# Performance work log

Measured on AMD Instinct MI355X. Metric: run time of the kernel, lower is better.

## Reference

```python
import jax, jax.numpy as jnp
import numpy as np

LEN = 2048

def setup_inputs() -> dict:
    key = jax.random.key(0)
    k1, k2 = jax.random.split(key)
    x = jax.random.normal(k1, (LEN,), dtype=jnp.float32)
    y = jax.random.normal(k2, (LEN,), dtype=jnp.float32)
    return {"x": x, "y": y}

def reference(x, y):
    # Classic DTW DP with squared-difference cost.
    # Original torch code clamps indices with max(i-1,0)/max(j-1,0); because
    # DTW[i,j] is still +inf when read, the clamped reads reduce to the
    # standard recurrence: row 0 is a cumulative sum, col 0 uses only 'up',
    # interior uses min(up, left, diag).
    inf = jnp.float32(jnp.inf)
    cost0 = (x[0] - y) ** 2            # [len2]
    row0 = jnp.cumsum(cost0)           # DTW row i=0

    def row_step(prev_row, xi):
        cost = (xi - y) ** 2                                   # [len2]
        diag = jnp.concatenate([prev_row[:1], prev_row[:-1]])  # prev_row[j-1], clamped at j=0
        def cell(left, cud):
            c, up, dg = cud
            v = c + jnp.minimum(jnp.minimum(up, left), dg)
            return v, v
        # left init = inf => at j=0 min reduces to min(up, diag) = prev_row[0]
        _, new_row = jax.lax.scan(cell, inf, (cost, prev_row, diag))
        return new_row, None

    last_row, _ = jax.lax.scan(row_step, row0, x[1:])
    return jnp.sqrt(last_row[-1])
```

## Files before the change

kernel.cpp:

```cpp
#include <hip/hip_runtime.h>
#include <math.h>


#define NLEN  2048
#define NW    4
#define CSTEP 64
#define DSKEW 128
#define PAD   64
#define RROW  (PAD + 2112)
#define GTOT  2496
#define INFV  1e30f

__device__ __forceinline__ float dpp_shr1(float v, float inj) {
    int r = __builtin_amdgcn_update_dpp(
        __builtin_bit_cast(int, inj), __builtin_bit_cast(int, v),
        0x138 , 0xF, 0xF, false );
    return __builtin_bit_cast(float, r);
}
__device__ __forceinline__ float rdlane(float v, int l) {
    return __builtin_bit_cast(float,
        __builtin_amdgcn_readlane(__builtin_bit_cast(int, v), l));
}
__device__ __forceinline__ float min3f(float a, float b, float c) {
    return fminf(fminf(a, b), c);
}

__global__ __launch_bounds__(256, 1) void dtw_kernel(const float* __restrict__ X,
                                                     const float* __restrict__ Y,
                                                     float* __restrict__ out) {
    __shared__ __align__(16) float yS[NLEN];
    __shared__ float ring[(NW + 1) * RROW];

    const int tid  = threadIdx.x;
    const int w    = tid >> 6;
    const int lane = tid & 63;

    {
        const float4* Y4 = (const float4*)Y;
        float4* y4 = (float4*)yS;
        y4[tid]       = Y4[tid];
        y4[tid + 256] = Y4[tid + 256];
    }
    for (int k = tid; k < (NW + 1) * RROW; k += 256) ring[k] = INFV;
    __syncthreads();

    float x0, x1, x2, x3, x4, x5, x6, x7;
    {
        const float4 xa = *(const float4*)&X[tid * 8];
        const float4 xb = *(const float4*)&X[tid * 8 + 4];
        x0 = xa.x; x1 = xa.y; x2 = xa.z; x3 = xa.w;
        x4 = xb.x; x5 = xb.y; x6 = xb.z; x7 = xb.w;
    }

    float v0 = INFV, v1 = INFV, v2 = INFV, v3 = INFV;
    float v4 = INFV, v5 = INFV, v6 = INFV, v7 = INFV;
    float uprev = (tid == 0) ? 0.0f : INFV;
    float yconv = 0.0f;

    const float* ringR = ring + w * RROW + PAD;
    float*       ringW = ring + (w + 1) * RROW + PAD;

    for (int gb = 0; gb < GTOT; gb += CSTEP) {
        const int tau0 = gb - w * DSKEW;

        if (tau0 >= 0 && tau0 <= NLEN) {
            int yi = tau0 + lane;
            if (yi >= NLEN) yi = NLEN - 1;
            const float yblk = yS[yi];
            const float rblk = ringR[tau0 + lane];
            float* wp = ringW + (tau0 - lane);
            const bool isout = (tau0 == NLEN) & (w == NW - 1) & (lane == 63);

            #pragma unroll
            for (int s = 0; s < CSTEP; ++s) {
                const float yu = rdlane(yblk, s);
                const float ru = rdlane(rblk, s);
                yconv = dpp_shr1(yconv, yu);
                const float u = dpp_shr1(v7, ru);
                float d0 = x0 - yconv; float nv0 = fmaf(d0, d0, min3f(v0, uprev, u));
                float d1 = x1 - yconv; float nv1 = fmaf(d1, d1, min3f(v1, v0, nv0));
                float d2 = x2 - yconv; float nv2 = fmaf(d2, d2, min3f(v2, v1, nv1));
                float d3 = x3 - yconv; float nv3 = fmaf(d3, d3, min3f(v3, v2, nv2));
                float d4 = x4 - yconv; float nv4 = fmaf(d4, d4, min3f(v4, v3, nv3));
                float d5 = x5 - yconv; float nv5 = fmaf(d5, d5, min3f(v5, v4, nv4));
                float d6 = x6 - yconv; float nv6 = fmaf(d6, d6, min3f(v6, v5, nv5));
                float d7 = x7 - yconv; float nv7 = fmaf(d7, d7, min3f(v7, v6, nv6));
                wp[s] = nv7;
                uprev = u;
                v0 = nv0; v1 = nv1; v2 = nv2; v3 = nv3;
                v4 = nv4; v5 = nv5; v6 = nv6; v7 = nv7;
                if (s == 62 && isout) out[0] = sqrtf(nv7);
            }
        }
        __syncthreads();
    }
}

extern "C" void kernel_launch(void* const* d_in, const int* in_sizes, int n_in,
                              void* d_out, int out_size, void* d_ws, size_t ws_size,
                              hipStream_t stream) {
    const float* x = (const float*)d_in[0];
    const float* y = (const float*)d_in[1];
    (void)in_sizes; (void)n_in; (void)out_size; (void)d_ws; (void)ws_size;
    dtw_kernel<<<1, 256, 0, stream>>>(x, y, (float*)d_out);
}
```

Measured before the change: 197.5 us.

## Skew lower half of per-thread rows by one step and use v_min3

Each thread's 8-row strip is split so rows 4-7 run one step behind rows 0-3. They consume the row-3 result from the previous step, which shortens the serial dependency chain per wavefront step from 8 to 4 dependent cells. The ring write offsets, skew, padding and total step count are adjusted to cover the extra pipeline latency. min3 is forced to a single v_min3_f32 instruction through inline asm. The cost is more steps and extra registers.

After: 241.6 us. 1.22x slower.

```diff
diff --git a/kernel.cpp b/kernel.cpp
--- a/kernel.cpp
+++ b/kernel.cpp
@@ -5,10 +5,11 @@
 #define NLEN  2048
 #define NW    4
 #define CSTEP 64
-#define DSKEW 128
-#define PAD   64
-#define RROW  (PAD + 2112)
-#define GTOT  2496
+#define DSKEW 192
+#define PAD   128
+#define TAUMAX (NLEN + CSTEP)
+#define RROW  (PAD + NLEN + 2 * CSTEP)
+#define GTOT  (TAUMAX + (NW - 1) * DSKEW + CSTEP)
 #define INFV  1e30f
 
 __device__ __forceinline__ float dpp_shr1(float v, float inj) {
@@ -22,7 +23,9 @@
         __builtin_amdgcn_readlane(__builtin_bit_cast(int, v), l));
 }
 __device__ __forceinline__ float min3f(float a, float b, float c) {
-    return fminf(fminf(a, b), c);
+    float r;
+    asm("v_min3_f32 %0, %1, %2, %3" : "=v"(r) : "v"(a), "v"(b), "v"(c));
+    return r;
 }
 
 __global__ __launch_bounds__(256, 1) void dtw_kernel(const float* __restrict__ X,
@@ -55,7 +58,8 @@
     float v0 = INFV, v1 = INFV, v2 = INFV, v3 = INFV;
     float v4 = INFV, v5 = INFV, v6 = INFV, v7 = INFV;
     float uprev = (tid == 0) ? 0.0f : INFV;
-    float yconv = 0.0f;
+    float yc = 0.0f, yd = 0.0f;
+    float n3a = INFV, n3b = INFV;
 
     const float* ringR = ring + w * RROW + PAD;
     float*       ringW = ring + (w + 1) * RROW + PAD;
@@ -63,30 +67,33 @@
     for (int gb = 0; gb < GTOT; gb += CSTEP) {
         const int tau0 = gb - w * DSKEW;
 
-        if (tau0 >= 0 && tau0 <= NLEN) {
+        if (tau0 >= 0 && tau0 <= TAUMAX) {
             int yi = tau0 + lane;
             if (yi >= NLEN) yi = NLEN - 1;
             const float yblk = yS[yi];
             const float rblk = ringR[tau0 + lane];
-            float* wp = ringW + (tau0 - lane);
-            const bool isout = (tau0 == NLEN) & (w == NW - 1) & (lane == 63);
+            float* wp = ringW + (tau0 - 2 * lane - 1);
+            const bool isout = (tau0 == TAUMAX) & (w == NW - 1) & (lane == 63);
 
             #pragma unroll
             for (int s = 0; s < CSTEP; ++s) {
-                const float yu = rdlane(yblk, s);
-                const float ru = rdlane(rblk, s);
-                yconv = dpp_shr1(yconv, yu);
-                const float u = dpp_shr1(v7, ru);
-                float d0 = x0 - yconv; float nv0 = fmaf(d0, d0, min3f(v0, uprev, u));
-                float d1 = x1 - yconv; float nv1 = fmaf(d1, d1, min3f(v1, v0, nv0));
-                float d2 = x2 - yconv; float nv2 = fmaf(d2, d2, min3f(v2, v1, nv1));
-                float d3 = x3 - yconv; float nv3 = fmaf(d3, d3, min3f(v3, v2, nv2));
-                float d4 = x4 - yconv; float nv4 = fmaf(d4, d4, min3f(v4, v3, nv3));
-                float d5 = x5 - yconv; float nv5 = fmaf(d5, d5, min3f(v5, v4, nv4));
-                float d6 = x6 - yconv; float nv6 = fmaf(d6, d6, min3f(v6, v5, nv5));
-                float d7 = x7 - yconv; float nv7 = fmaf(d7, d7, min3f(v7, v6, nv6));
+                const float yu  = rdlane(yblk, s);
+                const float ru  = rdlane(rblk, s);
+                const float ycn = dpp_shr1(yd, yu);
+                const float u   = dpp_shr1(v7, ru);
+                const float yH  = yc;
+                float d0 = x0 - ycn; float nv0 = fmaf(d0, d0, min3f(v0, uprev, u));
+                float d1 = x1 - ycn; float nv1 = fmaf(d1, d1, min3f(v1, v0, nv0));
+                float d2 = x2 - ycn; float nv2 = fmaf(d2, d2, min3f(v2, v1, nv1));
+                float d3 = x3 - ycn; float nv3 = fmaf(d3, d3, min3f(v3, v2, nv2));
+                float d4 = x4 - yH;  float nv4 = fmaf(d4, d4, min3f(v4, n3b, n3a));
+                float d5 = x5 - yH;  float nv5 = fmaf(d5, d5, min3f(v5, v4, nv4));
+                float d6 = x6 - yH;  float nv6 = fmaf(d6, d6, min3f(v6, v5, nv5));
+                float d7 = x7 - yH;  float nv7 = fmaf(d7, d7, min3f(v7, v6, nv6));
                 wp[s] = nv7;
                 uprev = u;
+                yd = yc; yc = ycn;
+                n3b = n3a; n3a = nv3;
                 v0 = nv0; v1 = nv1; v2 = nv2; v3 = nv3;
                 v4 = nv4; v5 = nv5; v6 = nv6; v7 = nv7;
                 if (s == 62 && isout) out[0] = sqrtf(nv7);
```
